# Optimization experiments

Measured on AMD Instinct MI355X. Metric: run time of the kernel, lower is better.

## Reference

```python
import jax, jax.numpy as jnp
import numpy as np

B, N, DIM = 1, 4096, 512
HEADS, LOCAL_HEADS = 8, 4           # int(8*0.6)=4 local, 4 content
CONTENT_HEADS = HEADS - LOCAL_HEADS
HEAD_DIM = DIM // HEADS             # 64
WINDOW = 64                         # == H == W so window attention is well-formed
TOPK_RATIO = 0.2
SCALE = HEAD_DIM ** -0.5


def _window_partition(x, ws):
    Bb, H, W, C = x.shape
    pad_h = (ws - H % ws) % ws
    pad_w = (ws - W % ws) % ws
    x = jnp.pad(x, ((0, 0), (0, pad_h), (0, pad_w), (0, 0)))
    Hp, Wp = H + pad_h, W + pad_w
    x = x.reshape(Bb, Hp // ws, ws, Wp // ws, ws, C)
    win = x.transpose(0, 1, 3, 2, 4, 5).reshape(-1, ws, ws, C)
    return win, (Hp, Wp)


def _window_unpartition(win, ws, pad_hw, hw):
    Hp, Wp = pad_hw
    H, W = hw
    Bb = win.shape[0] // (Hp * Wp // ws // ws)
    x = win.reshape(Bb, Hp // ws, Wp // ws, ws, ws, -1)
    x = x.transpose(0, 1, 3, 2, 4, 5).reshape(Bb, Hp, Wp, -1)
    return x[:, :H, :W, :]


def setup_inputs() -> dict:
    key = jax.random.key(0)
    ks = jax.random.split(key, 12)
    s = 0.02
    f32 = jnp.float32
    ld = LOCAL_HEADS * HEAD_DIM      # 256
    cd = CONTENT_HEADS * HEAD_DIM    # 256
    return {
        'x': jax.random.normal(ks[0], (B, N, DIM), f32),
        'W_lqkv': jax.random.normal(ks[1], (DIM, 3 * ld), f32) * s,
        'b_lqkv': jnp.zeros((3 * ld,), f32),
        'W_cqkv': jax.random.normal(ks[2], (DIM, 3 * cd), f32) * s,
        'b_cqkv': jnp.zeros((3 * cd,), f32),
        'W_lproj': jax.random.normal(ks[3], (ld, DIM), f32) * s,
        'b_lproj': jnp.zeros((DIM,), f32),
        'W_cproj': jax.random.normal(ks[4], (cd, DIM), f32) * s,
        'b_cproj': jnp.zeros((DIM,), f32),
        'W_s1': jax.random.normal(ks[5], (DIM, DIM // 2), f32) * s,
        'b_s1': jnp.zeros((DIM // 2,), f32),
        'W_s2': jax.random.normal(ks[6], (DIM // 2, 1), f32) * s,
        'b_s2': jnp.zeros((1,), f32),
    }


def reference(x, W_lqkv, b_lqkv, W_cqkv, b_cqkv, W_lproj, b_lproj,
              W_cproj, b_cproj, W_s1, b_s1, W_s2, b_s2):
    Bb, Nn, C = x.shape
    H = W = int(np.sqrt(Nn))

    # ---- local (windowed) attention branch ----
    x_sp = x.reshape(Bb, H, W, C)
    x_win, pad_hw = _window_partition(x_sp, WINDOW)           # (Bw, ws, ws, C)
    Bw, Hw, Ww, _ = x_win.shape
    Nw = Hw * Ww
    xl = x_win.reshape(Bw, Nw, C)
    lqkv = (xl @ W_lqkv + b_lqkv).reshape(Bw, Nw, 3, LOCAL_HEADS, HEAD_DIM)
    lqkv = lqkv.transpose(2, 0, 3, 1, 4)                      # (3, Bw, h, Nw, d)
    lq, lk, lv = lqkv[0], lqkv[1], lqkv[2]
    lattn = jnp.einsum('bhqd,bhkd->bhqk', lq, lk) * SCALE
    lattn = jax.nn.softmax(lattn, axis=-1)
    lo = jnp.einsum('bhqk,bhkd->bhqd', lattn, lv)
    lo = lo.transpose(0, 2, 1, 3).reshape(Bw, Hw, Ww, LOCAL_HEADS * HEAD_DIM)
    lo = _window_unpartition(lo, WINDOW, pad_hw, (H, W)).reshape(Bb, Nn, -1)
    local_x = lo @ W_lproj + b_lproj

    # ---- saliency-gated content-based sparse attention branch ----
    h = jax.nn.gelu(x @ W_s1 + b_s1, approximate=False)
    scores = (h @ W_s2 + b_s2)[..., 0]                        # (B, N)
    K = max(1, int(Nn * TOPK_RATIO))
    _, idx = jax.lax.top_k(scores, K)                         # (B, K)
    mask = jnp.zeros((Bb, Nn), bool).at[jnp.arange(Bb)[:, None], idx].set(True)

    cqkv = (x @ W_cqkv + b_cqkv).reshape(Bb, Nn, 3, CONTENT_HEADS, HEAD_DIM)
    cqkv = cqkv.transpose(2, 0, 3, 1, 4)
    cq, ck, cv = cqkv[0], cqkv[1], cqkv[2]
    cattn = jnp.einsum('bhqd,bhkd->bhqk', cq, ck) * SCALE
    cattn = jnp.where(mask[:, None, None, :], cattn, -jnp.inf)
    cattn = jax.nn.softmax(cattn, axis=-1)
    co = jnp.einsum('bhqk,bhkd->bhqd', cattn, cv)
    co = co.transpose(0, 2, 1, 3).reshape(Bb, Nn, CONTENT_HEADS * HEAD_DIM)
    content_x = co @ W_cproj + b_cproj

    out = local_x + content_x
    attn = jnp.concatenate([lattn.mean(axis=1), cattn.mean(axis=1)], axis=1)
    return out, attn
```

## Files before the change

### kernel.cpp

```cpp
#include <hip/hip_runtime.h>

typedef __bf16 bf16;
typedef __bf16 bf16x8 __attribute__((ext_vector_type(8)));
typedef float  floatx4 __attribute__((ext_vector_type(4)));

__device__ __forceinline__ floatx4 mfma16(bf16x8 a, bf16x8 b, floatx4 c) {
    return __builtin_amdgcn_mfma_f32_16x16x32_bf16(a, b, c, 0, 0, 0);
}

__device__ __forceinline__ bf16x8 load_f32_as_bf16x8(const float* p) {
    float4 f0 = *(const float4*)p;
    float4 f1 = *(const float4*)(p + 4);
    bf16x8 a;
    a[0] = (bf16)f0.x; a[1] = (bf16)f0.y; a[2] = (bf16)f0.z; a[3] = (bf16)f0.w;
    a[4] = (bf16)f1.x; a[5] = (bf16)f1.y; a[6] = (bf16)f1.z; a[7] = (bf16)f1.w;
    return a;
}

__global__ void k_transpose(const float* __restrict__ src, bf16* __restrict__ dst,
                            int R, int C) {
    __shared__ float tile[32][33];
    int c0 = blockIdx.x * 32, r0 = blockIdx.y * 32;
    int tx = threadIdx.x, ty = threadIdx.y;
    for (int i = ty; i < 32; i += 8) {
        int r = r0 + i, c = c0 + tx;
        tile[i][tx] = (r < R && c < C) ? src[r * C + c] : 0.f;
    }
    __syncthreads();
    for (int i = ty; i < 32; i += 8) {
        int r = r0 + tx, c = c0 + i;
        if (r < R && c < C) dst[(size_t)c * R + r] = (bf16)tile[tx][i];
    }
}

__global__ __launch_bounds__(256) void k_qkv(
    const float* __restrict__ x,
    const bf16* __restrict__ WlT, const bf16* __restrict__ WcT,
    const float* __restrict__ b_l, const float* __restrict__ b_c,
    bf16* __restrict__ lq, bf16* __restrict__ lk, bf16* __restrict__ lvT,
    bf16* __restrict__ cq, bf16* __restrict__ ck, bf16* __restrict__ cv)
{
    const int tid = threadIdx.x;
    const int wave = tid >> 6, lane = tid & 63;
    const int ln15 = lane & 15, quad = lane >> 4;
    const int m0 = blockIdx.x * 64 + wave * 16;
    const int n0 = blockIdx.y * 64;

    floatx4 acc[4];
    for (int s = 0; s < 4; ++s) acc[s] = (floatx4){0.f, 0.f, 0.f, 0.f};

    for (int k0 = 0; k0 < 512; k0 += 32) {
        bf16x8 a = load_f32_as_bf16x8(x + (m0 + ln15) * 512 + k0 + quad * 8);
        for (int s = 0; s < 4; ++s) {
            int cg = n0 + s * 16 + ln15;
            const bf16* bt = (cg < 768) ? (WlT + cg * 512) : (WcT + (cg - 768) * 512);
            bf16x8 b = *(const bf16x8*)(bt + k0 + quad * 8);
            acc[s] = mfma16(a, b, acc[s]);
        }
    }

    for (int s = 0; s < 4; ++s) {
        int cg = n0 + s * 16 + ln15;
        for (int r = 0; r < 4; ++r) {
            int row = m0 + quad * 4 + r;
            float v = acc[s][r];
            if (cg < 768) {
                v += b_l[cg];
                int qkv = cg >> 8, hh = (cg >> 6) & 3, d = cg & 63;
                if (qkv == 0)      lq[(hh * 4096 + row) * 64 + d] = (bf16)(v * 0.125f);
                else if (qkv == 1) lk[(hh * 4096 + row) * 64 + d] = (bf16)v;
                else               lvT[(hh * 64 + d) * 4096 + row] = (bf16)v;
            } else {
                int c = cg - 768;
                v += b_c[c];
                int qkv = c >> 8, hh = (c >> 6) & 3, d = c & 63;
                if (qkv == 0)      cq[(hh * 4096 + row) * 64 + d] = (bf16)(v * 0.125f);
                else if (qkv == 1) ck[(hh * 4096 + row) * 64 + d] = (bf16)v;
                else               cv[(hh * 4096 + row) * 64 + d] = (bf16)v;
            }
        }
    }
}

__global__ __launch_bounds__(256) void k_scores(
    const float* __restrict__ x, const float* __restrict__ Ws1,
    const float* __restrict__ bs1, const float* __restrict__ Ws2,
    const float* __restrict__ bs2, float* __restrict__ scores)
{
    __shared__ float xs[4][512];
    int row0 = blockIdx.x * 4;
    int t = threadIdx.x;
    for (int i = t; i < 512; i += 256) {
        int r = i >> 7, k4 = (i & 127) * 4;
        *(float4*)&xs[r][k4] = *(const float4*)&x[(row0 + r) * 512 + k4];
    }
    __syncthreads();
    int r = t >> 6, cb = (t & 63) * 4;
    float acc[4] = {0.f, 0.f, 0.f, 0.f};
    #pragma unroll 4
    for (int k = 0; k < 512; ++k) {
        float a = xs[r][k];
        float4 w = *(const float4*)(Ws1 + k * 256 + cb);
        acc[0] = fmaf(a, w.x, acc[0]); acc[1] = fmaf(a, w.y, acc[1]);
        acc[2] = fmaf(a, w.z, acc[2]); acc[3] = fmaf(a, w.w, acc[3]);
    }
    float s = 0.f;
    for (int j = 0; j < 4; ++j) {
        float v = acc[j] + bs1[cb + j];
        float g = 0.5f * v * (1.0f + erff(v * 0.70710678118654752f));
        s = fmaf(g, Ws2[cb + j], s);
    }
    s += __shfl_xor(s, 1, 64);  s += __shfl_xor(s, 2, 64);
    s += __shfl_xor(s, 4, 64);  s += __shfl_xor(s, 8, 64);
    s += __shfl_xor(s, 16, 64); s += __shfl_xor(s, 32, 64);
    if ((t & 63) == 0) scores[row0 + r] = s + bs2[0];
}

__global__ __launch_bounds__(1024) void k_topk(const float* __restrict__ scores,
                                               int* __restrict__ sel, int* __restrict__ pos) {
    __shared__ unsigned ubuf[4096];
    __shared__ unsigned cga[2048], cgb[2048];
    __shared__ int bidx[1024];
    __shared__ int ctr, bctr, Bbin;
    int tid = threadIdx.x;
    if (tid == 0) { ctr = 0; bctr = 0; }
    for (int i = tid; i < 2048; i += 1024) cga[i] = 0u;
    __syncthreads();
    for (int i = tid; i < 4096; i += 1024) {
        unsigned s = __float_as_uint(scores[i]);
        unsigned u = (s & 0x80000000u) ? ~s : (s | 0x80000000u);
        ubuf[i] = u;
        pos[i] = -1;
        atomicAdd(&cga[u >> 21], 1u);
    }
    __syncthreads();
    unsigned* src = cga; unsigned* dst = cgb;
    for (int off = 1; off < 2048; off <<= 1) {
        for (int i = tid; i < 2048; i += 1024)
            dst[i] = src[i] + ((i + off < 2048) ? src[i + off] : 0u);
        __syncthreads();
        unsigned* tmp = src; src = dst; dst = tmp;
    }
    for (int b = tid; b < 2048; b += 1024) {
        unsigned ge = src[b];
        unsigned gt = (b < 2047) ? src[b + 1] : 0u;
        if (ge >= 819u && gt < 819u) Bbin = b;
    }
    __syncthreads();
    int B = Bbin;
    int countAbove = (B < 2047) ? (int)src[B + 1] : 0;
    int need = 819 - countAbove;
    for (int i = tid; i < 4096; i += 1024) {
        int b = (int)(ubuf[i] >> 21);
        if (b > B) {
            int slot = atomicAdd(&ctr, 1);
            sel[slot] = i;
            pos[i] = slot;
        } else if (b == B) {
            int ls = atomicAdd(&bctr, 1);
            if (ls < 1024) bidx[ls] = i;
        }
    }
    __syncthreads();
    int m = bctr;
    if (m <= 1024) {
        for (int e = tid; e < m; e += 1024) {
            int i = bidx[e];
            unsigned ui = ubuf[i];
            int rank = 0;
            for (int j = 0; j < m; ++j) {
                int ij = bidx[j];
                unsigned uj = ubuf[ij];
                rank += (uj > ui || (uj == ui && ij < i)) ? 1 : 0;
            }
            if (rank < need) { int slot = countAbove + rank; sel[slot] = i; pos[i] = slot; }
        }
    } else {
        for (int i = tid; i < 4096; i += 1024) {
            if ((int)(ubuf[i] >> 21) != B) continue;
            unsigned ui = ubuf[i];
            int rank = 0;
            for (int j = 0; j < 4096; ++j) {
                if ((int)(ubuf[j] >> 21) != B) continue;
                unsigned uj = ubuf[j];
                rank += (uj > ui || (uj == ui && j < i)) ? 1 : 0;
            }
            if (rank < need) { int slot = countAbove + rank; sel[slot] = i; pos[i] = slot; }
        }
    }
}

__global__ __launch_bounds__(256) void k_gather(
    const bf16* __restrict__ ck, const bf16* __restrict__ cv,
    const int* __restrict__ sel,
    bf16* __restrict__ ckg, bf16* __restrict__ cvgT)
{
    int g = blockIdx.x * 4 + (threadIdx.x >> 6);
    int d = threadIdx.x & 63;
    int hh = g / 896, r = g % 896;
    int src = (r < 819) ? sel[r] : -1;
    bf16 kv = (src >= 0) ? ck[(hh * 4096 + src) * 64 + d] : (bf16)0.0f;
    bf16 vv = (src >= 0) ? cv[(hh * 4096 + src) * 64 + d] : (bf16)0.0f;
    ckg[(hh * 896 + r) * 64 + d] = kv;
    cvgT[(hh * 64 + d) * 896 + r] = vv;
}

__global__ __launch_bounds__(256, 5) void k_pass2b(
    const bf16* __restrict__ lq, const bf16* __restrict__ lk, const bf16* __restrict__ lvT,
    const bf16* __restrict__ cq, const bf16* __restrict__ ckg, const bf16* __restrict__ cvgT,
    float* __restrict__ partOL,
    float* __restrict__ partOC,
    float* __restrict__ partSL,
    float* __restrict__ partSC)
{
    __shared__ __align__(16) bf16 pbuf[4][2][16 * 40];
    int wave = threadIdx.x >> 6, lane = threadIdx.x & 63;
    int ln15 = lane & 15, quad = lane >> 4;
    int m0 = blockIdx.x * 64 + wave * 16;
    int y = blockIdx.y;
    bool local = y < 32;
    int h     = local ? (y >> 3) : ((y - 32) >> 1);
    int split = local ? (y & 7) : ((y - 32) & 1);
    int NV    = local ? 4096 : 896;
    int kbeg  = local ? split * 512 : split * 448;
    int kcnt  = local ? 512 : 448;

    const bf16* Qh = (local ? lq : cq) + (h * 4096 + m0) * 64;
    const bf16* Kh = (local ? lk : ckg) + h * NV * 64;
    const bf16* Vh = (local ? lvT : cvgT) + h * 64 * NV;

    bf16x8 af0 = *(const bf16x8*)(Qh + ln15 * 64 + quad * 8);
    bf16x8 af1 = *(const bf16x8*)(Qh + ln15 * 64 + 32 + quad * 8);

    floatx4 o[4];
    #pragma unroll
    for (int ds = 0; ds < 4; ++ds) o[ds] = (floatx4){0.f, 0.f, 0.f, 0.f};
    float se[4] = {0.f, 0.f, 0.f, 0.f};

    for (int key0 = kbeg; key0 < kbeg + kcnt; key0 += 64) {
        #pragma unroll
        for (int c = 0; c < 2; ++c) {
            int kb = key0 + c * 32;
            bf16* pb = &pbuf[wave][c][0];
            #pragma unroll
            for (int s = 0; s < 2; ++s) {
                int kc = kb + s * 16;
                const bf16* krow = Kh + (kc + ln15) * 64;
                floatx4 z = mfma16(af1, *(const bf16x8*)(krow + 32 + quad * 8),
                            mfma16(af0, *(const bf16x8*)(krow + quad * 8),
                                   (floatx4){0.f, 0.f, 0.f, 0.f}));
                bool valid = local || (kc + ln15) < 819;
                #pragma unroll
                for (int r = 0; r < 4; ++r) {
                    float p = valid ? __expf(fminf(z[r], 60.f)) : 0.0f;
                    se[r] += p;
                    pb[(quad * 4 + r) * 40 + s * 16 + ln15] = (bf16)p;
                }
            }
        }
        #pragma unroll
        for (int c = 0; c < 2; ++c) {
            int kb = key0 + c * 32;
            bf16x8 ap = *(const bf16x8*)(&pbuf[wave][c][0] + ln15 * 40 + quad * 8);
            #pragma unroll
            for (int ds = 0; ds < 4; ++ds) {
                const bf16* vrow = Vh + (ds * 16 + ln15) * NV + kb + quad * 8;
                o[ds] = mfma16(ap, *(const bf16x8*)vrow, o[ds]);
            }
        }
    }

    float* ps = (local ? partSL : partSC) + (split * 4 + h) * 4096;
    #pragma unroll
    for (int r = 0; r < 4; ++r) {
        float s = se[r];
        s += __shfl_xor(s, 1, 64);
        s += __shfl_xor(s, 2, 64);
        s += __shfl_xor(s, 4, 64);
        s += __shfl_xor(s, 8, 64);
        if (ln15 == 0) ps[m0 + quad * 4 + r] = s;
    }

    float* ob = (local ? partOL : partOC) + (size_t)split * (4096 * 256);
    #pragma unroll
    for (int ds = 0; ds < 4; ++ds)
        for (int r = 0; r < 4; ++r)
            ob[(m0 + quad * 4 + r) * 256 + h * 64 + ds * 16 + ln15] = o[ds][r];
}

__global__ __launch_bounds__(256) void k_reduce2(
    const float* __restrict__ partOL, const float* __restrict__ partOC,
    const float* __restrict__ partSL, const float* __restrict__ partSC,
    float* __restrict__ lsum, float* __restrict__ lo, float* __restrict__ co)
{
    int t = threadIdx.x;
    int q0 = blockIdx.x * 4;
    int r = t >> 6, cc = (t & 63) * 4;
    int q = q0 + r;
    int h = cc >> 6;

    float sl = 0.f;
    #pragma unroll
    for (int s = 0; s < 8; ++s) sl += partSL[(s * 4 + h) * 4096 + q];
    float rll = 1.0f / fmaxf(sl, 1e-30f);
    float a0 = 0.f, a1 = 0.f, a2 = 0.f, a3 = 0.f;
    #pragma unroll
    for (int s = 0; s < 8; ++s) {
        float4 v = *(const float4*)(partOL + (size_t)s * 1048576 + q * 256 + cc);
        a0 += v.x; a1 += v.y; a2 += v.z; a3 += v.w;
    }
    *(float4*)(lo + q * 256 + cc) = (float4){a0 * rll, a1 * rll, a2 * rll, a3 * rll};

    float sc = partSC[h * 4096 + q] + partSC[(4 + h) * 4096 + q];
    float rlc = 1.0f / fmaxf(sc, 1e-30f);
    float4 v0 = *(const float4*)(partOC + q * 256 + cc);
    float4 v1 = *(const float4*)(partOC + 1048576 + q * 256 + cc);
    *(float4*)(co + q * 256 + cc) = (float4){(v0.x + v1.x) * rlc, (v0.y + v1.y) * rlc,
                                             (v0.z + v1.z) * rlc, (v0.w + v1.w) * rlc};

    if (t < 32) {
        int h8 = t >> 2, rr = t & 3, qq = q0 + rr;
        float s = 0.f;
        if (h8 < 4) {
            #pragma unroll
            for (int sp = 0; sp < 8; ++sp) s += partSL[(sp * 4 + h8) * 4096 + qq];
        } else {
            s = partSC[(h8 - 4) * 4096 + qq] + partSC[(4 + h8 - 4) * 4096 + qq];
        }
        lsum[h8 * 4096 + qq] = s;
    }
}

__global__ __launch_bounds__(256) void k_pass2a(
    const bf16* __restrict__ lq, const bf16* __restrict__ lk,
    const bf16* __restrict__ cq, const bf16* __restrict__ ckg,
    const float* __restrict__ lsum,
    float* __restrict__ attn_local,
    bf16* __restrict__ pcomp)
{
    int wave = threadIdx.x >> 6, lane = threadIdx.x & 63;
    int ln15 = lane & 15, quad = lane >> 4;
    int m0 = blockIdx.x * 64 + wave * 16;
    int y = blockIdx.y;
    bool local = y < 32;
    const bf16* Q  = local ? lq : cq;
    const bf16* Kt = local ? lk : ckg;
    int NV = local ? 4096 : 896;
    int kbeg = local ? y * 128 : (y - 32) * 128;
    int kend = kbeg + 128;
    int hbase = local ? 0 : 4;

    bf16x8 af[4][2];
    #pragma unroll
    for (int h2 = 0; h2 < 4; ++h2)
        for (int ks = 0; ks < 2; ++ks)
            af[h2][ks] = *(const bf16x8*)(Q + (h2 * 4096 + m0 + ln15) * 64 + ks * 32 + quad * 8);

    float rl[4][4];
    #pragma unroll
    for (int h2 = 0; h2 < 4; ++h2)
        for (int r = 0; r < 4; ++r)
            rl[h2][r] = 0.25f / fmaxf(lsum[(hbase + h2) * 4096 + m0 + quad * 4 + r], 1e-30f);

    for (int key0 = kbeg; key0 < kend; key0 += 32) {
        float pm[2][4] = {{0.f, 0.f, 0.f, 0.f}, {0.f, 0.f, 0.f, 0.f}};
        #pragma unroll
        for (int h2 = 0; h2 < 4; ++h2) {
            #pragma unroll
            for (int s = 0; s < 2; ++s) {
                int kc = key0 + s * 16;
                const bf16* krow = Kt + (h2 * NV + kc + ln15) * 64;
                floatx4 z = (floatx4){0.f, 0.f, 0.f, 0.f};
                z = mfma16(af[h2][0], *(const bf16x8*)(krow + quad * 8), z);
                z = mfma16(af[h2][1], *(const bf16x8*)(krow + 32 + quad * 8), z);
                bool valid = local || (kc + ln15) < 819;
                if (valid)
                    for (int r = 0; r < 4; ++r)
                        pm[s][r] += __expf(fminf(z[r], 60.f)) * rl[h2][r];
            }
        }
        if (local) {
            #pragma unroll
            for (int s = 0; s < 2; ++s)
                for (int r = 0; r < 4; ++r)
                    attn_local[(m0 + quad * 4 + r) * 4096 + key0 + s * 16 + ln15] = pm[s][r];
        } else {
            #pragma unroll
            for (int s = 0; s < 2; ++s) {
                int kc = key0 + s * 16 + ln15;
                if (kc < 832)
                    for (int r = 0; r < 4; ++r)
                        pcomp[(m0 + quad * 4 + r) * 832 + kc] = (bf16)(pm[s][r]);
            }
        }
    }
}

__global__ __launch_bounds__(256) void k_expand(const bf16* __restrict__ pcomp,
                                                const int* __restrict__ pos,
                                                float* __restrict__ attn_content) {
    int row = blockIdx.x;
    int c0 = threadIdx.x * 16;
    const bf16* prow = pcomp + row * 832;
    float vals[16];
    #pragma unroll
    for (int j = 0; j < 16; ++j) {
        int p = pos[c0 + j];
        vals[j] = (p >= 0) ? (float)prow[p] : 0.0f;
    }
    float* dst = attn_content + (size_t)row * 4096 + c0;
    *(float4*)(dst)      = (float4){vals[0], vals[1], vals[2], vals[3]};
    *(float4*)(dst + 4)  = (float4){vals[4], vals[5], vals[6], vals[7]};
    *(float4*)(dst + 8)  = (float4){vals[8], vals[9], vals[10], vals[11]};
    *(float4*)(dst + 12) = (float4){vals[12], vals[13], vals[14], vals[15]};
}

__global__ __launch_bounds__(256) void k_proj(
    const float* __restrict__ lo, const float* __restrict__ co,
    const bf16* __restrict__ WlpT, const bf16* __restrict__ WcpT,
    const float* __restrict__ bl, const float* __restrict__ bc,
    float* __restrict__ out)
{
    const int tid = threadIdx.x;
    const int wave = tid >> 6, lane = tid & 63;
    const int ln15 = lane & 15, quad = lane >> 4;
    const int m0 = blockIdx.x * 64 + wave * 16;
    const int n0 = blockIdx.y * 64;

    floatx4 acc[4];
    for (int s = 0; s < 4; ++s) acc[s] = (floatx4){0.f, 0.f, 0.f, 0.f};

    for (int k0 = 0; k0 < 256; k0 += 32) {
        bf16x8 al = load_f32_as_bf16x8(lo + (m0 + ln15) * 256 + k0 + quad * 8);
        bf16x8 ac = load_f32_as_bf16x8(co + (m0 + ln15) * 256 + k0 + quad * 8);
        for (int s = 0; s < 4; ++s) {
            int c = n0 + s * 16 + ln15;
            acc[s] = mfma16(al, *(const bf16x8*)(WlpT + c * 256 + k0 + quad * 8), acc[s]);
            acc[s] = mfma16(ac, *(const bf16x8*)(WcpT + c * 256 + k0 + quad * 8), acc[s]);
        }
    }
    for (int s = 0; s < 4; ++s) {
        int c = n0 + s * 16 + ln15;
        float bias = bl[c] + bc[c];
        for (int r = 0; r < 4; ++r)
            out[(m0 + quad * 4 + r) * 512 + c] = acc[s][r] + bias;
    }
}

#define OFF_WLQKVT  0L
#define OFF_WCQKVT  786432L
#define OFF_LQ      1572864L
#define OFF_LK      3670016L
#define OFF_LVT     5767168L
#define OFF_CQ      7864320L
#define OFF_CK      9961472L
#define OFF_CV      12058624L
#define OFF_PCOMP   9961472L
#define OFF_CKG     16777216L
#define OFF_CVGT    17235968L
#define OFF_WLPT    16777216L
#define OFF_WCPT    17039360L
#define OFF_SCORES  17694720L
#define OFF_SEL     17711104L
#define OFF_POS     17715200L
#define OFF_LSUM    17731584L
#define OFF_LO      17862656L
#define OFF_CO      22056960L
#define WS_TOTAL    26251264L

extern "C" void kernel_launch(void* const* d_in, const int* in_sizes, int n_in,
                              void* d_out, int out_size, void* d_ws, size_t ws_size,
                              hipStream_t stream) {
    if (ws_size < (size_t)WS_TOTAL) return;

    const float* x       = (const float*)d_in[0];
    const float* W_lqkv  = (const float*)d_in[1];
    const float* b_lqkv  = (const float*)d_in[2];
    const float* W_cqkv  = (const float*)d_in[3];
    const float* b_cqkv  = (const float*)d_in[4];
    const float* W_lproj = (const float*)d_in[5];
    const float* b_lproj = (const float*)d_in[6];
    const float* W_cproj = (const float*)d_in[7];
    const float* b_cproj = (const float*)d_in[8];
    const float* W_s1    = (const float*)d_in[9];
    const float* b_s1    = (const float*)d_in[10];
    const float* W_s2    = (const float*)d_in[11];
    const float* b_s2    = (const float*)d_in[12];

    char* ws = (char*)d_ws;
    bf16* WlqkvT  = (bf16*)(ws + OFF_WLQKVT);
    bf16* WcqkvT  = (bf16*)(ws + OFF_WCQKVT);
    bf16* lq    = (bf16*)(ws + OFF_LQ);
    bf16* lk    = (bf16*)(ws + OFF_LK);
    bf16* lvT   = (bf16*)(ws + OFF_LVT);
    bf16* cq    = (bf16*)(ws + OFF_CQ);
    bf16* ck    = (bf16*)(ws + OFF_CK);
    bf16* cv    = (bf16*)(ws + OFF_CV);
    bf16* pcomp = (bf16*)(ws + OFF_PCOMP);
    bf16* ckg   = (bf16*)(ws + OFF_CKG);
    bf16* cvgT  = (bf16*)(ws + OFF_CVGT);
    bf16* WlpT  = (bf16*)(ws + OFF_WLPT);
    bf16* WcpT  = (bf16*)(ws + OFF_WCPT);
    float* scores  = (float*)(ws + OFF_SCORES);
    int*   sel     = (int*)(ws + OFF_SEL);
    int*   pos     = (int*)(ws + OFF_POS);
    float* lsum    = (float*)(ws + OFF_LSUM);
    float* lo      = (float*)(ws + OFF_LO);
    float* co      = (float*)(ws + OFF_CO);

    float* outp = (float*)d_out;
    float* attn_local   = outp + 2097152;
    float* attn_content = attn_local + 4096 * 4096;
    float* partOL = attn_content;
    float* partOC = attn_content + 8388608;
    float* partSL = attn_content + 10485760;
    float* partSC = attn_content + 10616832;

    k_transpose<<<dim3(24, 16), dim3(32, 8), 0, stream>>>(W_lqkv, WlqkvT, 512, 768);
    k_transpose<<<dim3(24, 16), dim3(32, 8), 0, stream>>>(W_cqkv, WcqkvT, 512, 768);

    k_qkv<<<dim3(64, 24), 256, 0, stream>>>(x, WlqkvT, WcqkvT, b_lqkv, b_cqkv,
                                            lq, lk, lvT, cq, ck, cv);
    k_scores<<<1024, 256, 0, stream>>>(x, W_s1, b_s1, W_s2, b_s2, scores);
    k_topk<<<1, 1024, 0, stream>>>(scores, sel, pos);
    k_gather<<<896, 256, 0, stream>>>(ck, cv, sel, ckg, cvgT);
    k_pass2b<<<dim3(64, 40), 256, 0, stream>>>(lq, lk, lvT, cq, ckg, cvgT,
                                               partOL, partOC, partSL, partSC);
    k_reduce2<<<1024, 256, 0, stream>>>(partOL, partOC, partSL, partSC, lsum, lo, co);
    k_pass2a<<<dim3(64, 39), 256, 0, stream>>>(lq, lk, cq, ckg, lsum,
                                               attn_local, pcomp);
    k_transpose<<<dim3(16, 8), dim3(32, 8), 0, stream>>>(W_lproj, WlpT, 256, 512);
    k_transpose<<<dim3(16, 8), dim3(32, 8), 0, stream>>>(W_cproj, WcpT, 256, 512);
    k_expand<<<4096, 256, 0, stream>>>(pcomp, pos, attn_content);
    k_proj<<<dim3(64, 8), 256, 0, stream>>>(lo, co, WlpT, WcpT, b_lproj, b_cproj, outp);
}
```

Before: 660.4 us.

## Precast x to bf16 and transpose V via LDS tiles instead of strided stores

After: 648.9 us. Within noise of the previous version (-1.7%).

```diff
diff --git a/kernel.cpp b/kernel.cpp
--- a/kernel.cpp
+++ b/kernel.cpp
@@ -6,15 +6,6 @@
 
 __device__ __forceinline__ floatx4 mfma16(bf16x8 a, bf16x8 b, floatx4 c) {
     return __builtin_amdgcn_mfma_f32_16x16x32_bf16(a, b, c, 0, 0, 0);
-}
-
-__device__ __forceinline__ bf16x8 load_f32_as_bf16x8(const float* p) {
-    float4 f0 = *(const float4*)p;
-    float4 f1 = *(const float4*)(p + 4);
-    bf16x8 a;
-    a[0] = (bf16)f0.x; a[1] = (bf16)f0.y; a[2] = (bf16)f0.z; a[3] = (bf16)f0.w;
-    a[4] = (bf16)f1.x; a[5] = (bf16)f1.y; a[6] = (bf16)f1.z; a[7] = (bf16)f1.w;
-    return a;
 }
 
 __global__ void k_transpose(const float* __restrict__ src, bf16* __restrict__ dst,
@@ -33,11 +24,42 @@
     }
 }
 
+__global__ __launch_bounds__(256) void k_xcast(const float* __restrict__ x,
+                                               bf16* __restrict__ xb) {
+    int i = (blockIdx.x * 256 + threadIdx.x) * 8;
+    float4 f0 = *(const float4*)(x + i);
+    float4 f1 = *(const float4*)(x + i + 4);
+    bf16x8 a;
+    a[0] = (bf16)f0.x; a[1] = (bf16)f0.y; a[2] = (bf16)f0.z; a[3] = (bf16)f0.w;
+    a[4] = (bf16)f1.x; a[5] = (bf16)f1.y; a[6] = (bf16)f1.z; a[7] = (bf16)f1.w;
+    *(bf16x8*)(xb + i) = a;
+}
+
+__global__ __launch_bounds__(256) void k_vtr(const bf16* __restrict__ src,
+                                             bf16* __restrict__ dst, int R) {
+    __shared__ bf16 tile[64][66];
+    int t = threadIdx.x;
+    int tr = blockIdx.x, h = blockIdx.y;
+    const bf16* s = src + ((size_t)h * R + tr * 64) * 64;
+    #pragma unroll
+    for (int rr = 0; rr < 16; ++rr) {
+        int row = rr * 4 + (t >> 6);
+        tile[row][t & 63] = s[row * 64 + (t & 63)];
+    }
+    __syncthreads();
+    bf16* d = dst + (size_t)h * 64 * R + tr * 64;
+    #pragma unroll
+    for (int cc = 0; cc < 16; ++cc) {
+        int col = cc * 4 + (t >> 6);
+        d[(size_t)col * R + (t & 63)] = tile[t & 63][col];
+    }
+}
+
 __global__ __launch_bounds__(256) void k_qkv(
-    const float* __restrict__ x,
+    const bf16* __restrict__ xb,
     const bf16* __restrict__ WlT, const bf16* __restrict__ WcT,
     const float* __restrict__ b_l, const float* __restrict__ b_c,
-    bf16* __restrict__ lq, bf16* __restrict__ lk, bf16* __restrict__ lvT,
+    bf16* __restrict__ lq, bf16* __restrict__ lk, bf16* __restrict__ lv,
     bf16* __restrict__ cq, bf16* __restrict__ ck, bf16* __restrict__ cv)
 {
     const int tid = threadIdx.x;
@@ -50,7 +72,7 @@
     for (int s = 0; s < 4; ++s) acc[s] = (floatx4){0.f, 0.f, 0.f, 0.f};
 
     for (int k0 = 0; k0 < 512; k0 += 32) {
-        bf16x8 a = load_f32_as_bf16x8(x + (m0 + ln15) * 512 + k0 + quad * 8);
+        bf16x8 a = *(const bf16x8*)(xb + (m0 + ln15) * 512 + k0 + quad * 8);
         for (int s = 0; s < 4; ++s) {
             int cg = n0 + s * 16 + ln15;
             const bf16* bt = (cg < 768) ? (WlT + cg * 512) : (WcT + (cg - 768) * 512);
@@ -69,7 +91,7 @@
                 int qkv = cg >> 8, hh = (cg >> 6) & 3, d = cg & 63;
                 if (qkv == 0)      lq[(hh * 4096 + row) * 64 + d] = (bf16)(v * 0.125f);
                 else if (qkv == 1) lk[(hh * 4096 + row) * 64 + d] = (bf16)v;
-                else               lvT[(hh * 64 + d) * 4096 + row] = (bf16)v;
+                else               lv[(hh * 4096 + row) * 64 + d] = (bf16)v;
             } else {
                 int c = cg - 768;
                 v += b_c[c];
@@ -193,7 +215,7 @@
 __global__ __launch_bounds__(256) void k_gather(
     const bf16* __restrict__ ck, const bf16* __restrict__ cv,
     const int* __restrict__ sel,
-    bf16* __restrict__ ckg, bf16* __restrict__ cvgT)
+    bf16* __restrict__ ckg, bf16* __restrict__ cvg)
 {
     int g = blockIdx.x * 4 + (threadIdx.x >> 6);
     int d = threadIdx.x & 63;
@@ -202,7 +224,7 @@
     bf16 kv = (src >= 0) ? ck[(hh * 4096 + src) * 64 + d] : (bf16)0.0f;
     bf16 vv = (src >= 0) ? cv[(hh * 4096 + src) * 64 + d] : (bf16)0.0f;
     ckg[(hh * 896 + r) * 64 + d] = kv;
-    cvgT[(hh * 64 + d) * 896 + r] = vv;
+    cvg[(hh * 896 + r) * 64 + d] = vv;
 }
 
 __global__ __launch_bounds__(256, 5) void k_pass2b(
@@ -246,13 +268,14 @@
             for (int s = 0; s < 2; ++s) {
                 int kc = kb + s * 16;
                 const bf16* krow = Kh + (kc + ln15) * 64;
-                floatx4 z = mfma16(af1, *(const bf16x8*)(krow + 32 + quad * 8),
-                            mfma16(af0, *(const bf16x8*)(krow + quad * 8),
-                                   (floatx4){0.f, 0.f, 0.f, 0.f}));
+                floatx4 z0 = (floatx4){0.f, 0.f, 0.f, 0.f};
+                floatx4 z1 = (floatx4){0.f, 0.f, 0.f, 0.f};
+                z0 = mfma16(af0, *(const bf16x8*)(krow + quad * 8), z0);
+                z1 = mfma16(af1, *(const bf16x8*)(krow + 32 + quad * 8), z1);
                 bool valid = local || (kc + ln15) < 819;
                 #pragma unroll
                 for (int r = 0; r < 4; ++r) {
-                    float p = valid ? __expf(fminf(z[r], 60.f)) : 0.0f;
+                    float p = valid ? __expf(fminf(z0[r] + z1[r], 60.f)) : 0.0f;
                     se[r] += p;
                     pb[(quad * 4 + r) * 40 + s * 16 + ln15] = (bf16)p;
                 }
@@ -370,13 +393,14 @@
             for (int s = 0; s < 2; ++s) {
                 int kc = key0 + s * 16;
                 const bf16* krow = Kt + (h2 * NV + kc + ln15) * 64;
-                floatx4 z = (floatx4){0.f, 0.f, 0.f, 0.f};
-                z = mfma16(af[h2][0], *(const bf16x8*)(krow + quad * 8), z);
-                z = mfma16(af[h2][1], *(const bf16x8*)(krow + 32 + quad * 8), z);
+                floatx4 z0 = (floatx4){0.f, 0.f, 0.f, 0.f};
+                floatx4 z1 = (floatx4){0.f, 0.f, 0.f, 0.f};
+                z0 = mfma16(af[h2][0], *(const bf16x8*)(krow + quad * 8), z0);
+                z1 = mfma16(af[h2][1], *(const bf16x8*)(krow + 32 + quad * 8), z1);
                 bool valid = local || (kc + ln15) < 819;
                 if (valid)
                     for (int r = 0; r < 4; ++r)
-                        pm[s][r] += __expf(fminf(z[r], 60.f)) * rl[h2][r];
+                        pm[s][r] += __expf(fminf(z0[r] + z1[r], 60.f)) * rl[h2][r];
             }
         }
         if (local) {
@@ -431,8 +455,15 @@
     for (int s = 0; s < 4; ++s) acc[s] = (floatx4){0.f, 0.f, 0.f, 0.f};
 
     for (int k0 = 0; k0 < 256; k0 += 32) {
-        bf16x8 al = load_f32_as_bf16x8(lo + (m0 + ln15) * 256 + k0 + quad * 8);
-        bf16x8 ac = load_f32_as_bf16x8(co + (m0 + ln15) * 256 + k0 + quad * 8);
+        const float* lp = lo + (m0 + ln15) * 256 + k0 + quad * 8;
+        const float* cp = co + (m0 + ln15) * 256 + k0 + quad * 8;
+        float4 l0 = *(const float4*)lp, l1 = *(const float4*)(lp + 4);
+        float4 c0 = *(const float4*)cp, c1 = *(const float4*)(cp + 4);
+        bf16x8 al, ac;
+        al[0] = (bf16)l0.x; al[1] = (bf16)l0.y; al[2] = (bf16)l0.z; al[3] = (bf16)l0.w;
+        al[4] = (bf16)l1.x; al[5] = (bf16)l1.y; al[6] = (bf16)l1.z; al[7] = (bf16)l1.w;
+        ac[0] = (bf16)c0.x; ac[1] = (bf16)c0.y; ac[2] = (bf16)c0.z; ac[3] = (bf16)c0.w;
+        ac[4] = (bf16)c1.x; ac[5] = (bf16)c1.y; ac[6] = (bf16)c1.z; ac[7] = (bf16)c1.w;
         for (int s = 0; s < 4; ++s) {
             int c = n0 + s * 16 + ln15;
             acc[s] = mfma16(al, *(const bf16x8*)(WlpT + c * 256 + k0 + quad * 8), acc[s]);
@@ -507,6 +538,9 @@
     float* lsum    = (float*)(ws + OFF_LSUM);
     float* lo      = (float*)(ws + OFF_LO);
     float* co      = (float*)(ws + OFF_CO);
+    bf16*  xb      = (bf16*)(ws + OFF_LO);
+    bf16*  lv      = (bf16*)(ws + OFF_CO);
+    bf16*  cvg     = (bf16*)(ws + OFF_CO + 2097152);
 
     float* outp = (float*)d_out;
     float* attn_local   = outp + 2097152;
@@ -518,12 +552,15 @@
 
     k_transpose<<<dim3(24, 16), dim3(32, 8), 0, stream>>>(W_lqkv, WlqkvT, 512, 768);
     k_transpose<<<dim3(24, 16), dim3(32, 8), 0, stream>>>(W_cqkv, WcqkvT, 512, 768);
-
-    k_qkv<<<dim3(64, 24), 256, 0, stream>>>(x, WlqkvT, WcqkvT, b_lqkv, b_cqkv,
-                                            lq, lk, lvT, cq, ck, cv);
+    k_xcast<<<1024, 256, 0, stream>>>(x, xb);
+
+    k_qkv<<<dim3(64, 24), 256, 0, stream>>>(xb, WlqkvT, WcqkvT, b_lqkv, b_cqkv,
+                                            lq, lk, lv, cq, ck, cv);
+    k_vtr<<<dim3(64, 4), 256, 0, stream>>>(lv, lvT, 4096);
     k_scores<<<1024, 256, 0, stream>>>(x, W_s1, b_s1, W_s2, b_s2, scores);
     k_topk<<<1, 1024, 0, stream>>>(scores, sel, pos);
-    k_gather<<<896, 256, 0, stream>>>(ck, cv, sel, ckg, cvgT);
+    k_gather<<<896, 256, 0, stream>>>(ck, cv, sel, ckg, cvg);
+    k_vtr<<<dim3(14, 4), 256, 0, stream>>>(cvg, cvgT, 896);
     k_pass2b<<<dim3(64, 40), 256, 0, stream>>>(lq, lk, lvT, cq, ckg, cvgT,
                                                partOL, partOC, partSL, partSC);
     k_reduce2<<<1024, 256, 0, stream>>>(partOL, partOC, partSL, partSC, lsum, lo, co);
```
